# Performance work log

Hardware: AMD Instinct MI355X
Metric: run time of the kernel (lower is better)

## Reference

```python
import jax, jax.numpy as jnp
import numpy as np

B, S, E, H, V, C = 256, 20, 512, 512, 32000, 1000


def _lstm_step(x, h, c, W, U, b):
    # Keras LSTM, activation='relu', recurrent_activation='sigmoid', gate order i,f,c,o
    z = x @ W + h @ U + b  # (B, 4H)
    i, f, g, o = jnp.split(z, 4, axis=-1)
    i = jax.nn.sigmoid(i)
    f = jax.nn.sigmoid(f)
    g = jax.nn.relu(g)
    o = jax.nn.sigmoid(o)
    c_new = f * c + i * g
    h_new = o * jax.nn.relu(c_new)
    return h_new, c_new


def setup_inputs() -> dict:
    key = jax.random.key(0)
    ks = jax.random.split(key, 24)
    std = 0.05
    d_in1 = S * E + 2 * E  # flattened encoder output + word embed + speaker embed
    inp = {
        "encoded_output": jax.random.normal(ks[0], (B, S, E), jnp.float32),
        "word_embedding": jax.random.normal(ks[1], (B, E), jnp.float32),
        "h0": jax.random.normal(ks[2], (B, H), jnp.float32) * std,
        "c0": jax.random.normal(ks[3], (B, H), jnp.float32) * std,
        "speaker": jax.random.randint(ks[4], (B,), 0, C),
        "addressee": jax.random.randint(ks[5], (B,), 0, C),
        "persona_emb": jax.random.normal(ks[6], (C, E), jnp.float32) * 0.1,
        "W1": jax.random.normal(ks[7], (d_in1, 4 * H), jnp.float32) * std,
        "U1": jax.random.normal(ks[8], (H, 4 * H), jnp.float32) * std,
        "b1": jnp.zeros((4 * H,), jnp.float32),
        "W2": jax.random.normal(ks[9], (H, 4 * H), jnp.float32) * std,
        "U2": jax.random.normal(ks[10], (H, 4 * H), jnp.float32) * std,
        "b2": jnp.zeros((4 * H,), jnp.float32),
        "W3": jax.random.normal(ks[11], (H, 4 * H), jnp.float32) * std,
        "U3": jax.random.normal(ks[12], (H, 4 * H), jnp.float32) * std,
        "b3": jnp.zeros((4 * H,), jnp.float32),
        "W4": jax.random.normal(ks[13], (H, 4 * H), jnp.float32) * std,
        "U4": jax.random.normal(ks[14], (H, 4 * H), jnp.float32) * std,
        "b4": jnp.zeros((4 * H,), jnp.float32),
        "Wd": jax.random.normal(ks[15], (H, V), jnp.float32) * std,
        "bd": jnp.zeros((V,), jnp.float32),
    }
    return inp


def reference(encoded_output, word_embedding, h0, c0, speaker, addressee,
              persona_emb, W1, U1, b1, W2, U2, b2, W3, U3, b3, W4, U4, b4, Wd, bd):
    b = encoded_output.shape[0]
    # The Python double loop in the original is exactly: (B,S,E) -> (B, S*E)
    enc_flat = encoded_output.reshape(b, -1)
    speaker_embed = persona_emb[speaker]  # (B, E)
    # is_speaker=True branch: concat [flattened encoder, word embed, speaker embed]
    x = jnp.concatenate([enc_flat, word_embedding, speaker_embed], axis=-1)
    # seq length is 1, so each LSTM layer is a single cell step;
    # each layer's initial state is the previous layer's final (h, c)
    h1, c1 = _lstm_step(x, h0, c0, W1, U1, b1)
    h2, c2 = _lstm_step(h1, h1, c1, W2, U2, b2)
    h3, c3 = _lstm_step(h2, h2, c2, W3, U3, b3)
    h4, c4 = _lstm_step(h3, h3, c3, W4, U4, b4)
    probs = jax.nn.softmax(h4 @ Wd + bd, axis=-1)  # (B, V)
    return probs, (h4, c4)
```

## Files before the change

kernel.cpp:

```cpp
#include <hip/hip_runtime.h>
#include <cstdint>
#include <cmath>

typedef _Float16 f16;
typedef _Float16 f16x8 __attribute__((ext_vector_type(8)));
typedef float f32x4 __attribute__((ext_vector_type(4)));

__device__ inline void gld_lds16(const void* g, void* l) {
  __builtin_amdgcn_global_load_lds(
      (__attribute__((address_space(1))) void*)(uintptr_t)g,
      (__attribute__((address_space(3))) void*)l, 16, 0, 0);
}

__global__ __launch_bounds__(256) void build_x1_kernel(
    const float* __restrict__ enc, const float* __restrict__ word,
    const float* __restrict__ pers, const int* __restrict__ speaker,
    const float* __restrict__ h0, f16* __restrict__ X)
{
  const int b  = blockIdx.y;
  const int k2 = blockIdx.x * 256 + threadIdx.x;
  const int k  = k2 * 2;
  float v0, v1;
  if (k < 10240) {
    const float* p = enc + (long long)b * 10240 + k; v0 = p[0]; v1 = p[1];
  } else if (k < 10752) {
    const float* p = word + b * 512 + (k - 10240);   v0 = p[0]; v1 = p[1];
  } else if (k < 11264) {
    const float* p = pers + (long long)speaker[b] * 512 + (k - 10752); v0 = p[0]; v1 = p[1];
  } else {
    const float* p = h0 + b * 512 + (k - 11264);     v0 = p[0]; v1 = p[1];
  }
  union { f16 h[2]; unsigned int u; } pk;
  pk.h[0] = (f16)v0; pk.h[1] = (f16)v1;
  ((unsigned int*)X)[(long long)b * 5888 + k2] = pk.u;
}

__global__ __launch_bounds__(256) void wsum_t_kernel(
    const float* __restrict__ W2, const float* __restrict__ U2,
    const float* __restrict__ W3, const float* __restrict__ U3,
    const float* __restrict__ W4, const float* __restrict__ U4,
    f16* __restrict__ out)
{
  const int t = blockIdx.x * 256 + threadIdx.x;
  const int L = blockIdx.y;
  const float* W = (L == 0) ? W2 : (L == 1) ? W3 : W4;
  const float* U = (L == 0) ? U2 : (L == 1) ? U3 : U4;
  const int n  = t & 2047;
  const int k0 = (t >> 11) << 6;
  f16* op = out + (long long)L * (2048 * 512) + (long long)n * 512 + k0;
  for (int kk = 0; kk < 64; kk += 8) {
    f16x8 v;
    #pragma unroll
    for (int j = 0; j < 8; j++) {
      const int k = k0 + kk + j;
      v[j] = (f16)(W[(long long)k * 2048 + n] + U[(long long)k * 2048 + n]);
    }
    *(f16x8*)(op + kk) = v;
  }
}

__global__ __launch_bounds__(256, 2) void gemm_f16_pipe(
    const f16* __restrict__ A, int lda,
    const float* __restrict__ B0, const float* __restrict__ B1, int ksw, int ldb,
    void* __restrict__ Cv, int ldc, long long c_split_stride, int niter,
    int store_f16)
{
  __shared__ __align__(16) f16 Ah[2][128 * 32];
  __shared__ __align__(16) f16 Bh[2][128 * 40];

  const int tid  = threadIdx.x;
  const int lane = tid & 63;
  const int wave = tid >> 6;
  const int m0 = blockIdx.x * 128;
  const int n0 = blockIdx.y * 128;
  const int kbeg = blockIdx.z * (niter * 32);

  const int a_row16 = lane >> 2;
  const int a_ksub  = ((lane & 3) ^ ((lane >> 3) & 3)) * 8;

  const int nl0  = (tid & 63) * 2;
  const int koct = tid >> 6;

  float2 bv[8];

  auto issueB = [&](int kt) {
    const int kb = kbeg + kt * 32 + koct * 8;
    #pragma unroll
    for (int i = 0; i < 8; i++) {
      const int krow = kb + i;
      const float* bp = (krow >= ksw) ? (B1 + (long long)(krow - ksw) * ldb)
                                      : (B0 + (long long)krow * ldb);
      bv[i] = *(const float2*)(bp + n0 + nl0);
    }
  };
  auto issueA = [&](int kt) {
    const int akb = kbeg + kt * 32;
    #pragma unroll
    for (int half = 0; half < 2; half++) {
      const int rb = wave * 32 + half * 16;
      const f16* gp = A + (long long)(m0 + rb + a_row16) * lda + akb + a_ksub;
      gld_lds16((const void*)gp, (void*)&Ah[kt & 1][rb * 32]);
    }
  };
  auto writeB = [&](int kt) {
    f16x8 p0, p1;
    #pragma unroll
    for (int i = 0; i < 8; i++) { p0[i] = (f16)bv[i].x; p1[i] = (f16)bv[i].y; }
    *(f16x8*)&Bh[kt & 1][(nl0    ) * 40 + koct * 8] = p0;
    *(f16x8*)&Bh[kt & 1][(nl0 + 1) * 40 + koct * 8] = p1;
  };

  const int wm = (wave & 1) * 64;
  const int wn = (wave >> 1) * 64;
  f32x4 acc[4][4] = {};

  issueB(0); issueA(0); writeB(0);
  __syncthreads();

  for (int kt = 0; kt < niter; kt++) {
    const int buf = kt & 1;
    const bool more = (kt + 1 < niter);
    if (more) { issueB(kt + 1); issueA(kt + 1); }

    f16x8 af[4], bf[4];
    #pragma unroll
    for (int mi = 0; mi < 4; mi++) {
      const int m = wm + mi * 16 + (lane & 15);
      af[mi] = *(const f16x8*)&Ah[buf][m * 32 + (((lane >> 4) ^ ((m >> 1) & 3)) * 8)];
    }
    #pragma unroll
    for (int ni = 0; ni < 4; ni++) {
      const int n = wn + ni * 16 + (lane & 15);
      bf[ni] = *(const f16x8*)&Bh[buf][n * 40 + (lane >> 4) * 8];
    }
    #pragma unroll
    for (int mi = 0; mi < 4; mi++)
      #pragma unroll
      for (int ni = 0; ni < 4; ni++)
        acc[mi][ni] = __builtin_amdgcn_mfma_f32_16x16x32_f16(af[mi], bf[ni], acc[mi][ni], 0, 0, 0);

    if (more) writeB(kt + 1);
    __syncthreads();
  }

  if (store_f16) {
    f16* Cs = (f16*)Cv + (long long)blockIdx.z * c_split_stride;
    #pragma unroll
    for (int mi = 0; mi < 4; mi++) {
      const int r0 = m0 + wm + mi * 16 + (lane >> 4) * 4;
      #pragma unroll
      for (int ni = 0; ni < 4; ni++) {
        const int cc = n0 + wn + ni * 16 + (lane & 15);
        #pragma unroll
        for (int r = 0; r < 4; r++)
          Cs[(long long)(r0 + r) * ldc + cc] = (f16)acc[mi][ni][r];
      }
    }
  } else {
    float* Cs = (float*)Cv + (long long)blockIdx.z * c_split_stride;
    #pragma unroll
    for (int mi = 0; mi < 4; mi++) {
      const int r0 = m0 + wm + mi * 16 + (lane >> 4) * 4;
      #pragma unroll
      for (int ni = 0; ni < 4; ni++) {
        const int cc = n0 + wn + ni * 16 + (lane & 15);
        #pragma unroll
        for (int r = 0; r < 4; r++)
          Cs[(long long)(r0 + r) * ldc + cc] = acc[mi][ni][r];
      }
    }
  }
}

__global__ __launch_bounds__(64) void lstm_small_layer(
    const f16* __restrict__ h_in,
    const f16* __restrict__ WsT,
    const float* __restrict__ bias,
    const float* __restrict__ c_prev, float* __restrict__ c_out,
    f16* __restrict__ h16_out, float* __restrict__ h32_out)
{
  const int lane = threadIdx.x;
  const int wid  = blockIdx.x;
  const int jt = wid & 31, mt = wid >> 5;
  const int m0 = mt * 32, j0 = jt * 16;
  const int lj = lane & 15, quad = lane >> 4;

  const f16* Ab = h_in + (long long)(m0 + lj) * 512 + quad * 8;
  const f16* Bb = WsT + (long long)(j0 + lj) * 512 + quad * 8;
  const long long GS = 512LL * 512;

  f32x4 a00 = {}, a01 = {}, a02 = {}, a03 = {};
  f32x4 a10 = {}, a11 = {}, a12 = {}, a13 = {};

  f16x8 ca0 = *(const f16x8*)(Ab);
  f16x8 ca1 = *(const f16x8*)(Ab + 16 * 512);
  f16x8 cb0 = *(const f16x8*)(Bb);
  f16x8 cb1 = *(const f16x8*)(Bb + GS);
  f16x8 cb2 = *(const f16x8*)(Bb + 2 * GS);
  f16x8 cb3 = *(const f16x8*)(Bb + 3 * GS);

  #pragma unroll
  for (int kt = 0; kt < 16; kt++) {
    f16x8 na0 = ca0, na1 = ca1, nb0 = cb0, nb1 = cb1, nb2 = cb2, nb3 = cb3;
    if (kt < 15) {
      const int k = (kt + 1) * 32;
      na0 = *(const f16x8*)(Ab + k);
      na1 = *(const f16x8*)(Ab + 16 * 512 + k);
      nb0 = *(const f16x8*)(Bb + k);
      nb1 = *(const f16x8*)(Bb + GS + k);
      nb2 = *(const f16x8*)(Bb + 2 * GS + k);
      nb3 = *(const f16x8*)(Bb + 3 * GS + k);
    }
    a00 = __builtin_amdgcn_mfma_f32_16x16x32_f16(ca0, cb0, a00, 0, 0, 0);
    a01 = __builtin_amdgcn_mfma_f32_16x16x32_f16(ca0, cb1, a01, 0, 0, 0);
    a02 = __builtin_amdgcn_mfma_f32_16x16x32_f16(ca0, cb2, a02, 0, 0, 0);
    a03 = __builtin_amdgcn_mfma_f32_16x16x32_f16(ca0, cb3, a03, 0, 0, 0);
    a10 = __builtin_amdgcn_mfma_f32_16x16x32_f16(ca1, cb0, a10, 0, 0, 0);
    a11 = __builtin_amdgcn_mfma_f32_16x16x32_f16(ca1, cb1, a11, 0, 0, 0);
    a12 = __builtin_amdgcn_mfma_f32_16x16x32_f16(ca1, cb2, a12, 0, 0, 0);
    a13 = __builtin_amdgcn_mfma_f32_16x16x32_f16(ca1, cb3, a13, 0, 0, 0);
    ca0 = na0; ca1 = na1; cb0 = nb0; cb1 = nb1; cb2 = nb2; cb3 = nb3;
  }

  const float bi = bias[j0 + lj],        bfv = bias[512 + j0 + lj];
  const float bg = bias[1024 + j0 + lj], bo  = bias[1536 + j0 + lj];
  #pragma unroll
  for (int r = 0; r < 4; r++) {
    {
      const int m = m0 + quad * 4 + r;
      const int idx = m * 512 + j0 + lj;
      const float gi = 1.f / (1.f + expf(-(a00[r] + bi)));
      const float gf = 1.f / (1.f + expf(-(a01[r] + bfv)));
      const float gg = fmaxf(a02[r] + bg, 0.f);
      const float go = 1.f / (1.f + expf(-(a03[r] + bo)));
      const float cn = gf * c_prev[idx] + gi * gg;
      const float hn = go * fmaxf(cn, 0.f);
      c_out[idx] = cn;
      h16_out[idx] = (f16)hn;
      if (h32_out) h32_out[idx] = hn;
    }
    {
      const int m = m0 + 16 + quad * 4 + r;
      const int idx = m * 512 + j0 + lj;
      const float gi = 1.f / (1.f + expf(-(a10[r] + bi)));
      const float gf = 1.f / (1.f + expf(-(a11[r] + bfv)));
      const float gg = fmaxf(a12[r] + bg, 0.f);
      const float go = 1.f / (1.f + expf(-(a13[r] + bo)));
      const float cn = gf * c_prev[idx] + gi * gg;
      const float hn = go * fmaxf(cn, 0.f);
      c_out[idx] = cn;
      h16_out[idx] = (f16)hn;
      if (h32_out) h32_out[idx] = hn;
    }
  }
}

__global__ __launch_bounds__(256) void gate_kernel(
    const unsigned int* __restrict__ zbase, const float* __restrict__ bias,
    const float* __restrict__ c_prev, float* __restrict__ c_out,
    f16* __restrict__ h16_out)
{
  const int idx2 = blockIdx.x * 256 + threadIdx.x;
  const int b  = idx2 >> 8;
  const int j2 = idx2 & 255;
  const int j  = j2 * 2;
  float z[4][2];
  #pragma unroll
  for (int g = 0; g < 4; g++) { z[g][0] = bias[g * 512 + j]; z[g][1] = bias[g * 512 + j + 1]; }
  for (int s = 0; s < 16; s++) {
    const unsigned int* zp = zbase + s * 262144 + b * 1024;
    #pragma unroll
    for (int g = 0; g < 4; g++) {
      union { unsigned int u; f16 h[2]; } v;
      v.u = zp[g * 256 + j2];
      z[g][0] += (float)v.h[0];
      z[g][1] += (float)v.h[1];
    }
  }
  #pragma unroll
  for (int e = 0; e < 2; e++) {
    const float gi = 1.f / (1.f + expf(-z[0][e]));
    const float gf = 1.f / (1.f + expf(-z[1][e]));
    const float gg = fmaxf(z[2][e], 0.f);
    const float go = 1.f / (1.f + expf(-z[3][e]));
    const int idx = b * 512 + j + e;
    const float cn = gf * c_prev[idx] + gi * gg;
    const float hn = go * fmaxf(cn, 0.f);
    c_out[idx] = cn;
    h16_out[idx] = (f16)hn;
  }
}

__global__ __launch_bounds__(1024) void softmax_kernel(
    float* __restrict__ logits, const float* __restrict__ bd)
{
  const int row = blockIdx.x;
  const int t = threadIdx.x;
  float4* rp = (float4*)(logits + (long long)row * 32000);
  const float4* bp = (const float4*)bd;
  float4 l[8];
  float m = -1e30f;
  #pragma unroll
  for (int i = 0; i < 8; i++) {
    const int v = t + i * 1024;
    if (v < 8000) {
      float4 x = rp[v]; const float4 bb = bp[v];
      x.x += bb.x; x.y += bb.y; x.z += bb.z; x.w += bb.w;
      l[i] = x;
      m = fmaxf(m, fmaxf(fmaxf(x.x, x.y), fmaxf(x.z, x.w)));
    } else {
      l[i] = make_float4(-1e30f, -1e30f, -1e30f, -1e30f);
    }
  }
  #pragma unroll
  for (int off = 32; off > 0; off >>= 1) m = fmaxf(m, __shfl_xor(m, off, 64));
  __shared__ float redm[16];
  __shared__ float reds[16];
  const int w = t >> 6;
  if ((t & 63) == 0) redm[w] = m;
  __syncthreads();
  float bm = redm[0];
  #pragma unroll
  for (int i = 1; i < 16; i++) bm = fmaxf(bm, redm[i]);
  float s = 0.f;
  #pragma unroll
  for (int i = 0; i < 8; i++) {
    const float ex = expf(l[i].x - bm), ey = expf(l[i].y - bm);
    const float ez = expf(l[i].z - bm), ew = expf(l[i].w - bm);
    l[i] = make_float4(ex, ey, ez, ew);
    s += (ex + ey) + (ez + ew);
  }
  #pragma unroll
  for (int off = 32; off > 0; off >>= 1) s += __shfl_xor(s, off, 64);
  if ((t & 63) == 0) reds[w] = s;
  __syncthreads();
  float ts = 0.f;
  #pragma unroll
  for (int i = 0; i < 16; i++) ts += reds[i];
  const float inv = 1.0f / ts;
  #pragma unroll
  for (int i = 0; i < 8; i++) {
    const int v = t + i * 1024;
    if (v < 8000) {
      float4 x = l[i];
      x.x *= inv; x.y *= inv; x.z *= inv; x.w *= inv;
      rp[v] = x;
    }
  }
}

extern "C" void kernel_launch(void* const* d_in, const int* in_sizes, int n_in,
                              void* d_out, int out_size, void* d_ws, size_t ws_size,
                              hipStream_t stream) {
  const float* enc     = (const float*)d_in[0];
  const float* word    = (const float*)d_in[1];
  const float* h0      = (const float*)d_in[2];
  const float* c0      = (const float*)d_in[3];
  const int*   speaker = (const int*)d_in[4];
  const float* pers = (const float*)d_in[6];
  const float* W1 = (const float*)d_in[7];
  const float* U1 = (const float*)d_in[8];
  const float* b1 = (const float*)d_in[9];
  const float* W2 = (const float*)d_in[10];
  const float* U2 = (const float*)d_in[11];
  const float* b2 = (const float*)d_in[12];
  const float* W3 = (const float*)d_in[13];
  const float* U3 = (const float*)d_in[14];
  const float* b3 = (const float*)d_in[15];
  const float* W4 = (const float*)d_in[16];
  const float* U4 = (const float*)d_in[17];
  const float* b4 = (const float*)d_in[18];
  const float* Wd = (const float*)d_in[19];
  const float* bd = (const float*)d_in[20];

  float* out = (float*)d_out;
  f16*   zp16  = (f16*)d_out;
  f16*   X1h   = (f16*)((char*)d_out + 16777216);
  float* h4_out = out + 8192000;
  float* c4_out = out + 8192000 + 131072;

  f16*   hA   = (f16*)d_ws;
  f16*   hB   = (f16*)((char*)d_ws + 262144);
  f16*   hC   = (f16*)((char*)d_ws + 524288);
  float* cbuf = (float*)((char*)d_ws + 786432);
  f16*   WsT  = (f16*)((char*)d_ws + 2097152);

  const int BIG = 1 << 29;
  const long long LW = 2048LL * 512;

  build_x1_kernel<<<dim3(23, 256), 256, 0, stream>>>(enc, word, pers, speaker, h0, X1h);
  wsum_t_kernel<<<dim3(64, 3), 256, 0, stream>>>(W2, U2, W3, U3, W4, U4, WsT);

  gemm_f16_pipe<<<dim3(2, 16, 16), 256, 0, stream>>>(
      X1h, 11776, W1, U1, 11264, 2048, zp16, 2048, 524288LL, 23, 1);
  gate_kernel<<<dim3(256), 256, 0, stream>>>((const unsigned int*)zp16, b1, c0, cbuf, hA);

  lstm_small_layer<<<dim3(256), 64, 0, stream>>>(hA, WsT,          b2, cbuf, cbuf, hB, nullptr);
  lstm_small_layer<<<dim3(256), 64, 0, stream>>>(hB, WsT + LW,     b3, cbuf, cbuf, hA, nullptr);
  lstm_small_layer<<<dim3(256), 64, 0, stream>>>(hA, WsT + 2 * LW, b4, cbuf, c4_out, hC, h4_out);

  gemm_f16_pipe<<<dim3(2, 250, 1), 256, 0, stream>>>(
      hC, 512, Wd, Wd, BIG, 32000, out, 32000, 0LL, 16, 0);

  softmax_kernel<<<dim3(256), 1024, 0, stream>>>(out, bd);
}
```

Before: 340.0 us.

## Cover full batch per GEMM block so fp32 weights are read once

```diff
diff --git a/kernel.cpp b/kernel.cpp
--- a/kernel.cpp
+++ b/kernel.cpp
@@ -59,21 +59,20 @@
   }
 }
 
-__global__ __launch_bounds__(256, 2) void gemm_f16_pipe(
+__global__ __launch_bounds__(256, 2) void gemm_pipe2(
     const f16* __restrict__ A, int lda,
     const float* __restrict__ B0, const float* __restrict__ B1, int ksw, int ldb,
     void* __restrict__ Cv, int ldc, long long c_split_stride, int niter,
     int store_f16)
 {
-  __shared__ __align__(16) f16 Ah[2][128 * 32];
+  __shared__ __align__(16) f16 Ah[2][256 * 32];
   __shared__ __align__(16) f16 Bh[2][128 * 40];
 
   const int tid  = threadIdx.x;
   const int lane = tid & 63;
   const int wave = tid >> 6;
-  const int m0 = blockIdx.x * 128;
-  const int n0 = blockIdx.y * 128;
-  const int kbeg = blockIdx.z * (niter * 32);
+  const int n0 = blockIdx.x * 128;
+  const int kbeg = blockIdx.y * (niter * 32);
 
   const int a_row16 = lane >> 2;
   const int a_ksub  = ((lane & 3) ^ ((lane >> 3) & 3)) * 8;
@@ -96,9 +95,9 @@
   auto issueA = [&](int kt) {
     const int akb = kbeg + kt * 32;
     #pragma unroll
-    for (int half = 0; half < 2; half++) {
-      const int rb = wave * 32 + half * 16;
-      const f16* gp = A + (long long)(m0 + rb + a_row16) * lda + akb + a_ksub;
+    for (int half = 0; half < 4; half++) {
+      const int rb = wave * 64 + half * 16;
+      const f16* gp = A + (long long)(rb + a_row16) * lda + akb + a_ksub;
       gld_lds16((const void*)gp, (void*)&Ah[kt & 1][rb * 32]);
     }
   };
@@ -110,9 +109,9 @@
     *(f16x8*)&Bh[kt & 1][(nl0 + 1) * 40 + koct * 8] = p1;
   };
 
-  const int wm = (wave & 1) * 64;
+  const int wm = (wave & 1) * 128;
   const int wn = (wave >> 1) * 64;
-  f32x4 acc[4][4] = {};
+  f32x4 acc[8][4] = {};
 
   issueB(0); issueA(0); writeB(0);
   __syncthreads();
@@ -122,32 +121,30 @@
     const bool more = (kt + 1 < niter);
     if (more) { issueB(kt + 1); issueA(kt + 1); }
 
-    f16x8 af[4], bf[4];
-    #pragma unroll
-    for (int mi = 0; mi < 4; mi++) {
-      const int m = wm + mi * 16 + (lane & 15);
-      af[mi] = *(const f16x8*)&Ah[buf][m * 32 + (((lane >> 4) ^ ((m >> 1) & 3)) * 8)];
-    }
+    f16x8 bf[4];
     #pragma unroll
     for (int ni = 0; ni < 4; ni++) {
       const int n = wn + ni * 16 + (lane & 15);
       bf[ni] = *(const f16x8*)&Bh[buf][n * 40 + (lane >> 4) * 8];
     }
     #pragma unroll
-    for (int mi = 0; mi < 4; mi++)
+    for (int mi = 0; mi < 8; mi++) {
+      const int m = wm + mi * 16 + (lane & 15);
+      const f16x8 af = *(const f16x8*)&Ah[buf][m * 32 + (((lane >> 4) ^ ((m >> 1) & 3)) * 8)];
       #pragma unroll
       for (int ni = 0; ni < 4; ni++)
-        acc[mi][ni] = __builtin_amdgcn_mfma_f32_16x16x32_f16(af[mi], bf[ni], acc[mi][ni], 0, 0, 0);
+        acc[mi][ni] = __builtin_amdgcn_mfma_f32_16x16x32_f16(af, bf[ni], acc[mi][ni], 0, 0, 0);
+    }
 
     if (more) writeB(kt + 1);
     __syncthreads();
   }
 
   if (store_f16) {
-    f16* Cs = (f16*)Cv + (long long)blockIdx.z * c_split_stride;
-    #pragma unroll
-    for (int mi = 0; mi < 4; mi++) {
-      const int r0 = m0 + wm + mi * 16 + (lane >> 4) * 4;
+    f16* Cs = (f16*)Cv + (long long)blockIdx.y * c_split_stride;
+    #pragma unroll
+    for (int mi = 0; mi < 8; mi++) {
+      const int r0 = wm + mi * 16 + (lane >> 4) * 4;
       #pragma unroll
       for (int ni = 0; ni < 4; ni++) {
         const int cc = n0 + wn + ni * 16 + (lane & 15);
@@ -157,10 +154,10 @@
       }
     }
   } else {
-    float* Cs = (float*)Cv + (long long)blockIdx.z * c_split_stride;
-    #pragma unroll
-    for (int mi = 0; mi < 4; mi++) {
-      const int r0 = m0 + wm + mi * 16 + (lane >> 4) * 4;
+    float* Cs = (float*)Cv + (long long)blockIdx.y * c_split_stride;
+    #pragma unroll
+    for (int mi = 0; mi < 8; mi++) {
+      const int r0 = wm + mi * 16 + (lane >> 4) * 4;
       #pragma unroll
       for (int ni = 0; ni < 4; ni++) {
         const int cc = n0 + wn + ni * 16 + (lane & 15);
@@ -182,18 +179,16 @@
   const int lane = threadIdx.x;
   const int wid  = blockIdx.x;
   const int jt = wid & 31, mt = wid >> 5;
-  const int m0 = mt * 32, j0 = jt * 16;
+  const int m0 = mt * 16, j0 = jt * 16;
   const int lj = lane & 15, quad = lane >> 4;
 
   const f16* Ab = h_in + (long long)(m0 + lj) * 512 + quad * 8;
   const f16* Bb = WsT + (long long)(j0 + lj) * 512 + quad * 8;
   const long long GS = 512LL * 512;
 
-  f32x4 a00 = {}, a01 = {}, a02 = {}, a03 = {};
-  f32x4 a10 = {}, a11 = {}, a12 = {}, a13 = {};
-
-  f16x8 ca0 = *(const f16x8*)(Ab);
-  f16x8 ca1 = *(const f16x8*)(Ab + 16 * 512);
+  f32x4 g0 = {}, g1 = {}, g2 = {}, g3 = {};
+
+  f16x8 ca = *(const f16x8*)(Ab);
   f16x8 cb0 = *(const f16x8*)(Bb);
   f16x8 cb1 = *(const f16x8*)(Bb + GS);
   f16x8 cb2 = *(const f16x8*)(Bb + 2 * GS);
@@ -201,62 +196,43 @@
 
   #pragma unroll
   for (int kt = 0; kt < 16; kt++) {
-    f16x8 na0 = ca0, na1 = ca1, nb0 = cb0, nb1 = cb1, nb2 = cb2, nb3 = cb3;
+    f16x8 na = ca, nb0 = cb0, nb1 = cb1, nb2 = cb2, nb3 = cb3;
     if (kt < 15) {
       const int k = (kt + 1) * 32;
-      na0 = *(const f16x8*)(Ab + k);
-      na1 = *(const f16x8*)(Ab + 16 * 512 + k);
+      na  = *(const f16x8*)(Ab + k);
       nb0 = *(const f16x8*)(Bb + k);
       nb1 = *(const f16x8*)(Bb + GS + k);
       nb2 = *(const f16x8*)(Bb + 2 * GS + k);
       nb3 = *(const f16x8*)(Bb + 3 * GS + k);
     }
-    a00 = __builtin_amdgcn_mfma_f32_16x16x32_f16(ca0, cb0, a00, 0, 0, 0);
-    a01 = __builtin_amdgcn_mfma_f32_16x16x32_f16(ca0, cb1, a01, 0, 0, 0);
-    a02 = __builtin_amdgcn_mfma_f32_16x16x32_f16(ca0, cb2, a02, 0, 0, 0);
-    a03 = __builtin_amdgcn_mfma_f32_16x16x32_f16(ca0, cb3, a03, 0, 0, 0);
-    a10 = __builtin_amdgcn_mfma_f32_16x16x32_f16(ca1, cb0, a10, 0, 0, 0);
-    a11 = __builtin_amdgcn_mfma_f32_16x16x32_f16(ca1, cb1, a11, 0, 0, 0);
-    a12 = __builtin_amdgcn_mfma_f32_16x16x32_f16(ca1, cb2, a12, 0, 0, 0);
-    a13 = __builtin_amdgcn_mfma_f32_16x16x32_f16(ca1, cb3, a13, 0, 0, 0);
-    ca0 = na0; ca1 = na1; cb0 = nb0; cb1 = nb1; cb2 = nb2; cb3 = nb3;
+    g0 = __builtin_amdgcn_mfma_f32_16x16x32_f16(ca, cb0, g0, 0, 0, 0);
+    g1 = __builtin_amdgcn_mfma_f32_16x16x32_f16(ca, cb1, g1, 0, 0, 0);
+    g2 = __builtin_amdgcn_mfma_f32_16x16x32_f16(ca, cb2, g2, 0, 0, 0);
+    g3 = __builtin_amdgcn_mfma_f32_16x16x32_f16(ca, cb3, g3, 0, 0, 0);
+    ca = na; cb0 = nb0; cb1 = nb1; cb2 = nb2; cb3 = nb3;
   }
 
   const float bi = bias[j0 + lj],        bfv = bias[512 + j0 + lj];
   const float bg = bias[1024 + j0 + lj], bo  = bias[1536 + j0 + lj];
   #pragma unroll
   for (int r = 0; r < 4; r++) {
-    {
-      const int m = m0 + quad * 4 + r;
-      const int idx = m * 512 + j0 + lj;
-      const float gi = 1.f / (1.f + expf(-(a00[r] + bi)));
-      const float gf = 1.f / (1.f + expf(-(a01[r] + bfv)));
-      const float gg = fmaxf(a02[r] + bg, 0.f);
-      const float go = 1.f / (1.f + expf(-(a03[r] + bo)));
-      const float cn = gf * c_prev[idx] + gi * gg;
-      const float hn = go * fmaxf(cn, 0.f);
-      c_out[idx] = cn;
-      h16_out[idx] = (f16)hn;
-      if (h32_out) h32_out[idx] = hn;
-    }
-    {
-      const int m = m0 + 16 + quad * 4 + r;
-      const int idx = m * 512 + j0 + lj;
-      const float gi = 1.f / (1.f + expf(-(a10[r] + bi)));
-      const float gf = 1.f / (1.f + expf(-(a11[r] + bfv)));
-      const float gg = fmaxf(a12[r] + bg, 0.f);
-      const float go = 1.f / (1.f + expf(-(a13[r] + bo)));
-      const float cn = gf * c_prev[idx] + gi * gg;
-      const float hn = go * fmaxf(cn, 0.f);
-      c_out[idx] = cn;
-      h16_out[idx] = (f16)hn;
-      if (h32_out) h32_out[idx] = hn;
-    }
+    const int m = m0 + quad * 4 + r;
+    const int idx = m * 512 + j0 + lj;
+    const float gi = 1.f / (1.f + expf(-(g0[r] + bi)));
+    const float gf = 1.f / (1.f + expf(-(g1[r] + bfv)));
+    const float gg = fmaxf(g2[r] + bg, 0.f);
+    const float go = 1.f / (1.f + expf(-(g3[r] + bo)));
+    const float cn = gf * c_prev[idx] + gi * gg;
+    const float hn = go * fmaxf(cn, 0.f);
+    c_out[idx] = cn;
+    h16_out[idx] = (f16)hn;
+    if (h32_out) h32_out[idx] = hn;
   }
 }
 
 __global__ __launch_bounds__(256) void gate_kernel(
-    const unsigned int* __restrict__ zbase, const float* __restrict__ bias,
+    const unsigned int* __restrict__ zbase, int nsplit,
+    const float* __restrict__ bias,
     const float* __restrict__ c_prev, float* __restrict__ c_out,
     f16* __restrict__ h16_out)
 {
@@ -267,8 +243,8 @@
   float z[4][2];
   #pragma unroll
   for (int g = 0; g < 4; g++) { z[g][0] = bias[g * 512 + j]; z[g][1] = bias[g * 512 + j + 1]; }
-  for (int s = 0; s < 16; s++) {
-    const unsigned int* zp = zbase + s * 262144 + b * 1024;
+  for (int s = 0; s < nsplit; s++) {
+    const unsigned int* zp = zbase + (long long)s * 262144 + b * 1024;
     #pragma unroll
     for (int g = 0; g < 4; g++) {
       union { unsigned int u; f16 h[2]; } v;
@@ -374,8 +350,6 @@
   const float* bd = (const float*)d_in[20];
 
   float* out = (float*)d_out;
-  f16*   zp16  = (f16*)d_out;
-  f16*   X1h   = (f16*)((char*)d_out + 16777216);
   float* h4_out = out + 8192000;
   float* c4_out = out + 8192000 + 131072;
 
@@ -384,6 +358,8 @@
   f16*   hC   = (f16*)((char*)d_ws + 524288);
   float* cbuf = (float*)((char*)d_ws + 786432);
   f16*   WsT  = (f16*)((char*)d_ws + 2097152);
+  f16*   X1h  = (f16*)((char*)d_ws + 8388608);
+  f16*   zp16 = (f16*)((char*)d_ws + 16777216);
 
   const int BIG = 1 << 29;
   const long long LW = 2048LL * 512;
@@ -391,15 +367,15 @@
   build_x1_kernel<<<dim3(23, 256), 256, 0, stream>>>(enc, word, pers, speaker, h0, X1h);
   wsum_t_kernel<<<dim3(64, 3), 256, 0, stream>>>(W2, U2, W3, U3, W4, U4, WsT);
 
-  gemm_f16_pipe<<<dim3(2, 16, 16), 256, 0, stream>>>(
-      X1h, 11776, W1, U1, 11264, 2048, zp16, 2048, 524288LL, 23, 1);
-  gate_kernel<<<dim3(256), 256, 0, stream>>>((const unsigned int*)zp16, b1, c0, cbuf, hA);
-
-  lstm_small_layer<<<dim3(256), 64, 0, stream>>>(hA, WsT,          b2, cbuf, cbuf, hB, nullptr);
-  lstm_small_layer<<<dim3(256), 64, 0, stream>>>(hB, WsT + LW,     b3, cbuf, cbuf, hA, nullptr);
-  lstm_small_layer<<<dim3(256), 64, 0, stream>>>(hA, WsT + 2 * LW, b4, cbuf, c4_out, hC, h4_out);
-
-  gemm_f16_pipe<<<dim3(2, 250, 1), 256, 0, stream>>>(
+  gemm_pipe2<<<dim3(16, 23), 256, 0, stream>>>(
+      X1h, 11776, W1, U1, 11264, 2048, zp16, 2048, 524288LL, 16, 1);
+  gate_kernel<<<dim3(256), 256, 0, stream>>>((const unsigned int*)zp16, 23, b1, c0, cbuf, hA);
+
+  lstm_small_layer<<<dim3(512), 64, 0, stream>>>(hA, WsT,          b2, cbuf, cbuf, hB, nullptr);
+  lstm_small_layer<<<dim3(512), 64, 0, stream>>>(hB, WsT + LW,     b3, cbuf, cbuf, hA, nullptr);
+  lstm_small_layer<<<dim3(512), 64, 0, stream>>>(hA, WsT + 2 * LW, b4, cbuf, c4_out, hC, h4_out);
+
+  gemm_pipe2<<<dim3(250, 1), 256, 0, stream>>>(
       hC, 512, Wd, Wd, BIG, 32000, out, 32000, 0LL, 16, 0);
 
   softmax_kernel<<<dim3(256), 1024, 0, stream>>>(out, bd);
```

Measured after the change: 335.7 us. No clear change (-1.3%).
